# Optimization experiments

Measured on AMD Instinct MI355X. Metric: run time of the kernel, lower is better.

Reference implementation:

```python
import jax, jax.numpy as jnp
import numpy as np

RMS_EPS = 1e-5
L2_EPS = 1e-8


def _rms_norm(x, eps=RMS_EPS):
    return x * jax.lax.rsqrt(jnp.mean(x * x, axis=-1, keepdims=True) + eps)


def _l2_norm(x, eps=L2_EPS):
    return jnp.linalg.norm(x, ord=2, axis=-1, keepdims=True) + eps


def setup_inputs() -> dict:
    key = jax.random.key(0)
    kq, kk, kv = jax.random.split(key, 3)
    B, H, S, D = 4, 16, 4096, 64
    Q = jax.random.normal(kq, (B, H, S, D), dtype=jnp.float32)
    K = jax.random.normal(kk, (B, H, S, D), dtype=jnp.float32)
    V = jax.random.normal(kv, (B, H, S, D), dtype=jnp.float32)
    return {"Q": Q, "K": K, "V": V}


def reference(Q, K, V):
    # v_swiglu = SiLU(V) * V
    v_swiglu = jax.nn.silu(V) * V
    # causal cumulative sum over sequence dim
    c = jnp.cumsum(v_swiglu, axis=-2)
    c_n = _rms_norm(c)
    # gating scalar per (b,h,s): ||Q|| + ||K|| + 1
    r = _l2_norm(Q) + _l2_norm(K) + 1.0
    mstate = c_n / r
    # SwiGLU combine: V + SiLU(mstate) * V, then final RMSNorm
    out0 = V + jax.nn.silu(mstate) * V
    return _rms_norm(out0)
```

## Files before the change

kernel.cpp:

```cpp
#include <hip/hip_runtime.h>
#include <math.h>

#define BH 64
#define SEQ 4096
#define DIM 64
#define CHUNK 32
#define NCHUNK (SEQ / CHUNK)
#define WPB 4

__device__ __forceinline__ float fast_rcp(float x)  { return __builtin_amdgcn_rcpf(x); }
__device__ __forceinline__ float fast_rsqrt(float x){ return __builtin_amdgcn_rsqf(x); }
__device__ __forceinline__ float fast_sigmoid(float x) {
    return fast_rcp(1.0f + __expf(-x));
}


__global__ __launch_bounds__(256) void k_partials(const float* __restrict__ Q,
                                                  const float* __restrict__ K,
                                                  const float* __restrict__ V,
                                                  float* __restrict__ P,
                                                  float* __restrict__ R) {
    const int wave  = threadIdx.x >> 6;
    const int lane  = threadIdx.x & 63;
    const int g     = lane >> 4;
    const int h     = lane & 15;
    const int chunk = blockIdx.x * WPB + wave;

    const size_t cbase = (size_t)chunk * (CHUNK * DIM);
    const float4* q4 = (const float4*)(Q + cbase);
    const float4* k4 = (const float4*)(K + cbase);
    const float4* v4 = (const float4*)(V + cbase);

    float acc0 = 0.f, acc1 = 0.f, acc2 = 0.f, acc3 = 0.f;

#pragma unroll
    for (int j0 = 0; j0 < CHUNK; j0 += 4) {
        const int row = j0 + g;
        const int idx = row * 16 + h;
        float4 q = q4[idx];
        float4 k = k4[idx];
        float4 v = v4[idx];

        float q2 = q.x*q.x + q.y*q.y + q.z*q.z + q.w*q.w;
        float k2 = k.x*k.x + k.y*k.y + k.z*k.z + k.w*k.w;
#pragma unroll
        for (int m = 1; m < 16; m <<= 1) {
            q2 += __shfl_xor(q2, m);
            k2 += __shfl_xor(k2, m);
        }
        float r = sqrtf(q2) + sqrtf(k2) + 1.0f;
        if (h == 0) R[(size_t)chunk * CHUNK + row] = r;

        acc0 += v.x * v.x * fast_sigmoid(v.x);
        acc1 += v.y * v.y * fast_sigmoid(v.y);
        acc2 += v.z * v.z * fast_sigmoid(v.z);
        acc3 += v.w * v.w * fast_sigmoid(v.w);
    }

#pragma unroll
    for (int m = 16; m < 64; m <<= 1) {
        acc0 += __shfl_xor(acc0, m);
        acc1 += __shfl_xor(acc1, m);
        acc2 += __shfl_xor(acc2, m);
        acc3 += __shfl_xor(acc3, m);
    }
    if (g == 0) {
        float4 out = {acc0, acc1, acc2, acc3};
        ((float4*)(P + (size_t)chunk * DIM))[h] = out;
    }
}

__global__ __launch_bounds__(256) void k_prefix(float* __restrict__ P) {
    __shared__ float seg[WPB][DIM];
    const int wave = threadIdx.x >> 6;
    const int lane = threadIdx.x & 63;
    const int bh   = blockIdx.x;
    const int SEG  = NCHUNK / WPB;

    float* p = P + (size_t)bh * (NCHUNK * DIM) + (size_t)wave * SEG * DIM + lane;

    float t[SEG];
#pragma unroll
    for (int i = 0; i < SEG; ++i) t[i] = p[i * DIM];

    float run = 0.f;
#pragma unroll
    for (int i = 0; i < SEG; ++i) { float x = t[i]; t[i] = run; run += x; }

    seg[wave][lane] = run;
    __syncthreads();

    float carry = 0.f;
#pragma unroll
    for (int w = 0; w < WPB; ++w)
        if (w < wave) carry += seg[w][lane];

#pragma unroll
    for (int i = 0; i < SEG; ++i) p[i * DIM] = t[i] + carry;
}

__global__ __launch_bounds__(256) void k_scan(const float* __restrict__ V,
                                              const float* __restrict__ P,
                                              const float* __restrict__ R,
                                              float* __restrict__ O) {
    const int wave  = threadIdx.x >> 6;
    const int lane  = threadIdx.x & 63;
    const int g     = lane >> 4;
    const int h     = lane & 15;
    const int chunk = blockIdx.x * WPB + wave;

    const size_t cbase = (size_t)chunk * (CHUNK * DIM);
    const float4* v4 = (const float4*)(V + cbase);
    float4*       o4 = (float4*)(O + cbase);
    const float*  rp = R + (size_t)chunk * CHUNK;

    float4 cb = ((const float4*)(P + (size_t)chunk * DIM))[h];
    float c_base[4] = {cb.x, cb.y, cb.z, cb.w};

    const int up16 = (lane + 48) & 63;
    const int up32 = (lane + 32) & 63;
    const int src3 = 48 + h;

#pragma unroll
    for (int j0 = 0; j0 < CHUNK; j0 += 4) {
        const int row = j0 + g;
        float4 v = v4[row * 16 + h];

        float sw[4];
        sw[0] = v.x * v.x * fast_sigmoid(v.x);
        sw[1] = v.y * v.y * fast_sigmoid(v.y);
        sw[2] = v.z * v.z * fast_sigmoid(v.z);
        sw[3] = v.w * v.w * fast_sigmoid(v.w);

#pragma unroll
        for (int i = 0; i < 4; ++i) {
            float t = __shfl(sw[i], up16);
            sw[i] += (g >= 1) ? t : 0.f;
        }
#pragma unroll
        for (int i = 0; i < 4; ++i) {
            float t = __shfl(sw[i], up32);
            sw[i] += (g >= 2) ? t : 0.f;
        }

        float c_row[4], tot[4];
#pragma unroll
        for (int i = 0; i < 4; ++i) {
            tot[i]   = __shfl(sw[i], src3);
            c_row[i] = c_base[i] + sw[i];
            c_base[i] += tot[i];
        }

        float c2 = c_row[0]*c_row[0] + c_row[1]*c_row[1]
                 + c_row[2]*c_row[2] + c_row[3]*c_row[3];
#pragma unroll
        for (int m = 1; m < 16; m <<= 1) c2 += __shfl_xor(c2, m);

        float r     = rp[row];
        float rms_c = fast_rsqrt(c2 * (1.0f / 64.0f) + 1e-5f);
        float s     = rms_c * fast_rcp(r);

        float vv[4] = {v.x, v.y, v.z, v.w};
        float o[4];
#pragma unroll
        for (int i = 0; i < 4; ++i) {
            float m_ = c_row[i] * s;
            o[i] = vv[i] * (1.0f + m_ * fast_sigmoid(m_));
        }

        float o2 = o[0]*o[0] + o[1]*o[1] + o[2]*o[2] + o[3]*o[3];
#pragma unroll
        for (int m = 1; m < 16; m <<= 1) o2 += __shfl_xor(o2, m);

        float rms_o = fast_rsqrt(o2 * (1.0f / 64.0f) + 1e-5f);
        float4 out = {o[0]*rms_o, o[1]*rms_o, o[2]*rms_o, o[3]*rms_o};
        o4[row * 16 + h] = out;
    }
}

extern "C" void kernel_launch(void* const* d_in, const int* in_sizes, int n_in,
                              void* d_out, int out_size, void* d_ws, size_t ws_size,
                              hipStream_t stream) {
    const float* Q = (const float*)d_in[0];
    const float* K = (const float*)d_in[1];
    const float* V = (const float*)d_in[2];
    float* O = (float*)d_out;
    float* P = (float*)d_ws;
    float* R = (float*)d_ws + (size_t)BH * NCHUNK * DIM;

    const int nchunks = BH * NCHUNK;
    k_partials<<<nchunks / WPB, 256, 0, stream>>>(Q, K, V, P, R);
    k_prefix<<<BH, 256, 0, stream>>>(P);
    k_scan<<<nchunks / WPB, 256, 0, stream>>>(V, P, R, O);
}
```

Baseline: 234.5 us.

## Fuse three-pass scan into persistent kernel with grid barriers

Replaces the partials, prefix and scan kernels with one persistent kernel of 256 blocks that uses two atomic grid-wide barriers between phases. Each wave handles several chunks. The Q/K norm computation moves from the partials pass into the final pass, so the R buffer round trip goes away and Q/K are read only once. The aim is to remove kernel launch gaps and the R traffic. In exchange it adds a memset, spin-wait barriers that rely on all 256 blocks being co-resident, and less parallelism per phase.

```diff
diff --git a/kernel.cpp b/kernel.cpp
--- a/kernel.cpp
+++ b/kernel.cpp
@@ -6,7 +6,12 @@
 #define DIM 64
 #define CHUNK 32
 #define NCHUNK (SEQ / CHUNK)
-#define WPB 4
+#define TPB 512
+#define WPB 8
+#define BLOCKS 256
+#define TOTAL_WAVES (BLOCKS * WPB)
+#define CPW ((BH * NCHUNK) / TOTAL_WAVES)
+#define PFX_SEG (NCHUNK / WPB)
 
 __device__ __forceinline__ float fast_rcp(float x)  { return __builtin_amdgcn_rcpf(x); }
 __device__ __forceinline__ float fast_rsqrt(float x){ return __builtin_amdgcn_rsqf(x); }
@@ -14,167 +19,172 @@
     return fast_rcp(1.0f + __expf(-x));
 }
 
-
-__global__ __launch_bounds__(256) void k_partials(const float* __restrict__ Q,
+__device__ __forceinline__ void grid_barrier(int* cnt, int* flag) {
+    __syncthreads();
+    __threadfence();
+    if (threadIdx.x == 0) {
+        int prev = atomicAdd(cnt, 1);
+        if (prev == BLOCKS - 1) {
+            atomicExch(flag, 1);
+        } else {
+            while (atomicAdd(flag, 0) == 0) {
+                __builtin_amdgcn_s_sleep(8);
+            }
+        }
+    }
+    __syncthreads();
+    __threadfence();
+}
+
+__global__ __launch_bounds__(TPB, 4) void k_fused(const float* __restrict__ Q,
                                                   const float* __restrict__ K,
                                                   const float* __restrict__ V,
                                                   float* __restrict__ P,
-                                                  float* __restrict__ R) {
-    const int wave  = threadIdx.x >> 6;
-    const int lane  = threadIdx.x & 63;
-    const int g     = lane >> 4;
-    const int h     = lane & 15;
-    const int chunk = blockIdx.x * WPB + wave;
-
-    const size_t cbase = (size_t)chunk * (CHUNK * DIM);
-    const float4* q4 = (const float4*)(Q + cbase);
-    const float4* k4 = (const float4*)(K + cbase);
-    const float4* v4 = (const float4*)(V + cbase);
-
-    float acc0 = 0.f, acc1 = 0.f, acc2 = 0.f, acc3 = 0.f;
-
-#pragma unroll
-    for (int j0 = 0; j0 < CHUNK; j0 += 4) {
-        const int row = j0 + g;
-        const int idx = row * 16 + h;
-        float4 q = q4[idx];
-        float4 k = k4[idx];
-        float4 v = v4[idx];
-
-        float q2 = q.x*q.x + q.y*q.y + q.z*q.z + q.w*q.w;
-        float k2 = k.x*k.x + k.y*k.y + k.z*k.z + k.w*k.w;
-#pragma unroll
-        for (int m = 1; m < 16; m <<= 1) {
-            q2 += __shfl_xor(q2, m);
-            k2 += __shfl_xor(k2, m);
-        }
-        float r = sqrtf(q2) + sqrtf(k2) + 1.0f;
-        if (h == 0) R[(size_t)chunk * CHUNK + row] = r;
-
-        acc0 += v.x * v.x * fast_sigmoid(v.x);
-        acc1 += v.y * v.y * fast_sigmoid(v.y);
-        acc2 += v.z * v.z * fast_sigmoid(v.z);
-        acc3 += v.w * v.w * fast_sigmoid(v.w);
-    }
-
-#pragma unroll
-    for (int m = 16; m < 64; m <<= 1) {
-        acc0 += __shfl_xor(acc0, m);
-        acc1 += __shfl_xor(acc1, m);
-        acc2 += __shfl_xor(acc2, m);
-        acc3 += __shfl_xor(acc3, m);
-    }
-    if (g == 0) {
-        float4 out = {acc0, acc1, acc2, acc3};
-        ((float4*)(P + (size_t)chunk * DIM))[h] = out;
-    }
-}
-
-__global__ __launch_bounds__(256) void k_prefix(float* __restrict__ P) {
+                                                  float* __restrict__ O,
+                                                  int* __restrict__ bar) {
     __shared__ float seg[WPB][DIM];
+
     const int wave = threadIdx.x >> 6;
     const int lane = threadIdx.x & 63;
-    const int bh   = blockIdx.x;
-    const int SEG  = NCHUNK / WPB;
-
-    float* p = P + (size_t)bh * (NCHUNK * DIM) + (size_t)wave * SEG * DIM + lane;
-
-    float t[SEG];
-#pragma unroll
-    for (int i = 0; i < SEG; ++i) t[i] = p[i * DIM];
-
-    float run = 0.f;
-#pragma unroll
-    for (int i = 0; i < SEG; ++i) { float x = t[i]; t[i] = run; run += x; }
-
-    seg[wave][lane] = run;
-    __syncthreads();
-
-    float carry = 0.f;
-#pragma unroll
-    for (int w = 0; w < WPB; ++w)
-        if (w < wave) carry += seg[w][lane];
-
-#pragma unroll
-    for (int i = 0; i < SEG; ++i) p[i * DIM] = t[i] + carry;
-}
-
-__global__ __launch_bounds__(256) void k_scan(const float* __restrict__ V,
-                                              const float* __restrict__ P,
-                                              const float* __restrict__ R,
-                                              float* __restrict__ O) {
-    const int wave  = threadIdx.x >> 6;
-    const int lane  = threadIdx.x & 63;
-    const int g     = lane >> 4;
-    const int h     = lane & 15;
-    const int chunk = blockIdx.x * WPB + wave;
-
-    const size_t cbase = (size_t)chunk * (CHUNK * DIM);
-    const float4* v4 = (const float4*)(V + cbase);
-    float4*       o4 = (float4*)(O + cbase);
-    const float*  rp = R + (size_t)chunk * CHUNK;
-
-    float4 cb = ((const float4*)(P + (size_t)chunk * DIM))[h];
-    float c_base[4] = {cb.x, cb.y, cb.z, cb.w};
+    const int g    = lane >> 4;
+    const int h    = lane & 15;
+    const int wid  = blockIdx.x * WPB + wave;
+
+    for (int t = 0; t < CPW; ++t) {
+        const int chunk = wid * CPW + t;
+        const float4* v4 = (const float4*)(V + (size_t)chunk * (CHUNK * DIM));
+
+        float acc0 = 0.f, acc1 = 0.f, acc2 = 0.f, acc3 = 0.f;
+#pragma unroll
+        for (int j0 = 0; j0 < CHUNK; j0 += 4) {
+            float4 v = v4[(j0 + g) * 16 + h];
+            acc0 += v.x * v.x * fast_sigmoid(v.x);
+            acc1 += v.y * v.y * fast_sigmoid(v.y);
+            acc2 += v.z * v.z * fast_sigmoid(v.z);
+            acc3 += v.w * v.w * fast_sigmoid(v.w);
+        }
+#pragma unroll
+        for (int m = 16; m < 64; m <<= 1) {
+            acc0 += __shfl_xor(acc0, m);
+            acc1 += __shfl_xor(acc1, m);
+            acc2 += __shfl_xor(acc2, m);
+            acc3 += __shfl_xor(acc3, m);
+        }
+        if (g == 0) {
+            float4 out = {acc0, acc1, acc2, acc3};
+            ((float4*)(P + (size_t)chunk * DIM))[h] = out;
+        }
+    }
+
+    grid_barrier(bar + 0, bar + 1);
+
+    if (blockIdx.x < BH) {
+        const int bh = blockIdx.x;
+        float* p = P + (size_t)bh * (NCHUNK * DIM) + (size_t)wave * PFX_SEG * DIM + lane;
+
+        float tr[PFX_SEG];
+#pragma unroll
+        for (int i = 0; i < PFX_SEG; ++i) tr[i] = p[i * DIM];
+
+        float run = 0.f;
+#pragma unroll
+        for (int i = 0; i < PFX_SEG; ++i) { float x = tr[i]; tr[i] = run; run += x; }
+
+        seg[wave][lane] = run;
+        __syncthreads();
+
+        float carry = 0.f;
+#pragma unroll
+        for (int w = 0; w < WPB; ++w)
+            if (w < wave) carry += seg[w][lane];
+
+#pragma unroll
+        for (int i = 0; i < PFX_SEG; ++i) p[i * DIM] = tr[i] + carry;
+    }
+
+    grid_barrier(bar + 2, bar + 3);
 
     const int up16 = (lane + 48) & 63;
     const int up32 = (lane + 32) & 63;
     const int src3 = 48 + h;
 
-#pragma unroll
-    for (int j0 = 0; j0 < CHUNK; j0 += 4) {
-        const int row = j0 + g;
-        float4 v = v4[row * 16 + h];
-
-        float sw[4];
-        sw[0] = v.x * v.x * fast_sigmoid(v.x);
-        sw[1] = v.y * v.y * fast_sigmoid(v.y);
-        sw[2] = v.z * v.z * fast_sigmoid(v.z);
-        sw[3] = v.w * v.w * fast_sigmoid(v.w);
-
-#pragma unroll
-        for (int i = 0; i < 4; ++i) {
-            float t = __shfl(sw[i], up16);
-            sw[i] += (g >= 1) ? t : 0.f;
-        }
-#pragma unroll
-        for (int i = 0; i < 4; ++i) {
-            float t = __shfl(sw[i], up32);
-            sw[i] += (g >= 2) ? t : 0.f;
-        }
-
-        float c_row[4], tot[4];
-#pragma unroll
-        for (int i = 0; i < 4; ++i) {
-            tot[i]   = __shfl(sw[i], src3);
-            c_row[i] = c_base[i] + sw[i];
-            c_base[i] += tot[i];
-        }
-
-        float c2 = c_row[0]*c_row[0] + c_row[1]*c_row[1]
-                 + c_row[2]*c_row[2] + c_row[3]*c_row[3];
-#pragma unroll
-        for (int m = 1; m < 16; m <<= 1) c2 += __shfl_xor(c2, m);
-
-        float r     = rp[row];
-        float rms_c = fast_rsqrt(c2 * (1.0f / 64.0f) + 1e-5f);
-        float s     = rms_c * fast_rcp(r);
-
-        float vv[4] = {v.x, v.y, v.z, v.w};
-        float o[4];
-#pragma unroll
-        for (int i = 0; i < 4; ++i) {
-            float m_ = c_row[i] * s;
-            o[i] = vv[i] * (1.0f + m_ * fast_sigmoid(m_));
-        }
-
-        float o2 = o[0]*o[0] + o[1]*o[1] + o[2]*o[2] + o[3]*o[3];
-#pragma unroll
-        for (int m = 1; m < 16; m <<= 1) o2 += __shfl_xor(o2, m);
-
-        float rms_o = fast_rsqrt(o2 * (1.0f / 64.0f) + 1e-5f);
-        float4 out = {o[0]*rms_o, o[1]*rms_o, o[2]*rms_o, o[3]*rms_o};
-        o4[row * 16 + h] = out;
+    for (int t = 0; t < CPW; ++t) {
+        const int chunk = wid * CPW + t;
+        const size_t cbase = (size_t)chunk * (CHUNK * DIM);
+        const float4* q4 = (const float4*)(Q + cbase);
+        const float4* k4 = (const float4*)(K + cbase);
+        const float4* v4 = (const float4*)(V + cbase);
+        float4*       o4 = (float4*)(O + cbase);
+
+        float4 cb = ((const float4*)(P + (size_t)chunk * DIM))[h];
+        float c_base[4] = {cb.x, cb.y, cb.z, cb.w};
+
+#pragma unroll
+        for (int j0 = 0; j0 < CHUNK; j0 += 4) {
+            const int row = j0 + g;
+            const int idx = row * 16 + h;
+            float4 v = v4[idx];
+            float4 q = q4[idx];
+            float4 k = k4[idx];
+
+            float q2 = q.x*q.x + q.y*q.y + q.z*q.z + q.w*q.w;
+            float k2 = k.x*k.x + k.y*k.y + k.z*k.z + k.w*k.w;
+#pragma unroll
+            for (int m = 1; m < 16; m <<= 1) {
+                q2 += __shfl_xor(q2, m);
+                k2 += __shfl_xor(k2, m);
+            }
+            float r = sqrtf(q2) + sqrtf(k2) + 1.0f;
+
+            float sw[4];
+            sw[0] = v.x * v.x * fast_sigmoid(v.x);
+            sw[1] = v.y * v.y * fast_sigmoid(v.y);
+            sw[2] = v.z * v.z * fast_sigmoid(v.z);
+            sw[3] = v.w * v.w * fast_sigmoid(v.w);
+
+#pragma unroll
+            for (int i = 0; i < 4; ++i) {
+                float tt = __shfl(sw[i], up16);
+                sw[i] += (g >= 1) ? tt : 0.f;
+            }
+#pragma unroll
+            for (int i = 0; i < 4; ++i) {
+                float tt = __shfl(sw[i], up32);
+                sw[i] += (g >= 2) ? tt : 0.f;
+            }
+
+            float c_row[4];
+#pragma unroll
+            for (int i = 0; i < 4; ++i) {
+                float tot = __shfl(sw[i], src3);
+                c_row[i]  = c_base[i] + sw[i];
+                c_base[i] += tot;
+            }
+
+            float c2 = c_row[0]*c_row[0] + c_row[1]*c_row[1]
+                     + c_row[2]*c_row[2] + c_row[3]*c_row[3];
+#pragma unroll
+            for (int m = 1; m < 16; m <<= 1) c2 += __shfl_xor(c2, m);
+
+            float rms_c = fast_rsqrt(c2 * (1.0f / 64.0f) + 1e-5f);
+            float s     = rms_c * fast_rcp(r);
+
+            float vv[4] = {v.x, v.y, v.z, v.w};
+            float o[4];
+#pragma unroll
+            for (int i = 0; i < 4; ++i) {
+                float m_ = c_row[i] * s;
+                o[i] = vv[i] * (1.0f + m_ * fast_sigmoid(m_));
+            }
+
+            float o2 = o[0]*o[0] + o[1]*o[1] + o[2]*o[2] + o[3]*o[3];
+#pragma unroll
+            for (int m = 1; m < 16; m <<= 1) o2 += __shfl_xor(o2, m);
+
+            float rms_o = fast_rsqrt(o2 * (1.0f / 64.0f) + 1e-5f);
+            float4 out = {o[0]*rms_o, o[1]*rms_o, o[2]*rms_o, o[3]*rms_o};
+            o4[idx] = out;
+        }
     }
 }
 
@@ -186,10 +196,8 @@
     const float* V = (const float*)d_in[2];
     float* O = (float*)d_out;
     float* P = (float*)d_ws;
-    float* R = (float*)d_ws + (size_t)BH * NCHUNK * DIM;
-
-    const int nchunks = BH * NCHUNK;
-    k_partials<<<nchunks / WPB, 256, 0, stream>>>(Q, K, V, P, R);
-    k_prefix<<<BH, 256, 0, stream>>>(P);
-    k_scan<<<nchunks / WPB, 256, 0, stream>>>(V, P, R, O);
-}
+    int* bar = (int*)((char*)d_ws + (size_t)BH * NCHUNK * DIM * sizeof(float));
+
+    hipMemsetAsync(bar, 0, 4 * sizeof(int), stream);
+    k_fused<<<BLOCKS, TPB, 0, stream>>>(Q, K, V, P, O, bar);
+}
```

After: 371.2 us. 1.58x slower.

## Fuse prefix pass into scan kernel and move Q/K norm computation there

Applied to the files above, without the earlier changes.

Drops the separate prefix kernel: each scan block recomputes the chunk-prefix carry for its batch-head slab from the partial sums, using shared memory. The Q/K L2-norm gate is now computed inside the scan kernel instead of the partials kernel, so the R buffer round trip goes away and the partials pass reads only V. Each wave now handles two chunks, interleaved, to expose more memory-level parallelism, with launch bounds set for occupancy. The cost is redundant prefix reads of P in every block (16 blocks per slab) and more registers per thread.

```diff
diff --git a/kernel.cpp b/kernel.cpp
--- a/kernel.cpp
+++ b/kernel.cpp
@@ -6,7 +6,10 @@
 #define DIM 64
 #define CHUNK 32
 #define NCHUNK (SEQ / CHUNK)
-#define WPB 4
+#define NCH_TOT (BH * NCHUNK)
+#define P1_WPB 4
+#define CPB 8
+#define SBLOCKS (NCH_TOT / CPB)
 
 __device__ __forceinline__ float fast_rcp(float x)  { return __builtin_amdgcn_rcpf(x); }
 __device__ __forceinline__ float fast_rsqrt(float x){ return __builtin_amdgcn_rsqf(x); }
@@ -14,108 +17,161 @@
     return fast_rcp(1.0f + __expf(-x));
 }
 
+__device__ __forceinline__ float red16(float x) {
+    x += __shfl_xor(x, 1);
+    x += __shfl_xor(x, 2);
+    x += __shfl_xor(x, 4);
+    x += __shfl_xor(x, 8);
+    return x;
+}
 
-__global__ __launch_bounds__(256) void k_partials(const float* __restrict__ Q,
-                                                  const float* __restrict__ K,
-                                                  const float* __restrict__ V,
-                                                  float* __restrict__ P,
-                                                  float* __restrict__ R) {
-    const int wave  = threadIdx.x >> 6;
-    const int lane  = threadIdx.x & 63;
-    const int g     = lane >> 4;
-    const int h     = lane & 15;
-    const int chunk = blockIdx.x * WPB + wave;
+__global__ __launch_bounds__(256) void k_partials(const float* __restrict__ V,
+                                                  float* __restrict__ P) {
+    const int wave = threadIdx.x >> 6;
+    const int lane = threadIdx.x & 63;
+    const int g = lane >> 4, h = lane & 15;
+    const int chunk = blockIdx.x * P1_WPB + wave;
 
-    const size_t cbase = (size_t)chunk * (CHUNK * DIM);
-    const float4* q4 = (const float4*)(Q + cbase);
-    const float4* k4 = (const float4*)(K + cbase);
-    const float4* v4 = (const float4*)(V + cbase);
-
-    float acc0 = 0.f, acc1 = 0.f, acc2 = 0.f, acc3 = 0.f;
-
+    const float4* v4 = (const float4*)(V + (size_t)chunk * (CHUNK * DIM));
+    float a0 = 0.f, a1 = 0.f, a2 = 0.f, a3 = 0.f;
 #pragma unroll
     for (int j0 = 0; j0 < CHUNK; j0 += 4) {
-        const int row = j0 + g;
-        const int idx = row * 16 + h;
-        float4 q = q4[idx];
-        float4 k = k4[idx];
-        float4 v = v4[idx];
-
-        float q2 = q.x*q.x + q.y*q.y + q.z*q.z + q.w*q.w;
-        float k2 = k.x*k.x + k.y*k.y + k.z*k.z + k.w*k.w;
-#pragma unroll
-        for (int m = 1; m < 16; m <<= 1) {
-            q2 += __shfl_xor(q2, m);
-            k2 += __shfl_xor(k2, m);
-        }
-        float r = sqrtf(q2) + sqrtf(k2) + 1.0f;
-        if (h == 0) R[(size_t)chunk * CHUNK + row] = r;
-
-        acc0 += v.x * v.x * fast_sigmoid(v.x);
-        acc1 += v.y * v.y * fast_sigmoid(v.y);
-        acc2 += v.z * v.z * fast_sigmoid(v.z);
-        acc3 += v.w * v.w * fast_sigmoid(v.w);
+        float4 v = v4[(j0 + g) * 16 + h];
+        a0 += v.x * v.x * fast_sigmoid(v.x);
+        a1 += v.y * v.y * fast_sigmoid(v.y);
+        a2 += v.z * v.z * fast_sigmoid(v.z);
+        a3 += v.w * v.w * fast_sigmoid(v.w);
     }
-
 #pragma unroll
     for (int m = 16; m < 64; m <<= 1) {
-        acc0 += __shfl_xor(acc0, m);
-        acc1 += __shfl_xor(acc1, m);
-        acc2 += __shfl_xor(acc2, m);
-        acc3 += __shfl_xor(acc3, m);
+        a0 += __shfl_xor(a0, m);
+        a1 += __shfl_xor(a1, m);
+        a2 += __shfl_xor(a2, m);
+        a3 += __shfl_xor(a3, m);
     }
     if (g == 0) {
-        float4 out = {acc0, acc1, acc2, acc3};
-        ((float4*)(P + (size_t)chunk * DIM))[h] = out;
+        float4 o = {a0, a1, a2, a3};
+        ((float4*)(P + (size_t)chunk * DIM))[h] = o;
     }
 }
 
-__global__ __launch_bounds__(256) void k_prefix(float* __restrict__ P) {
-    __shared__ float seg[WPB][DIM];
-    const int wave = threadIdx.x >> 6;
-    const int lane = threadIdx.x & 63;
-    const int bh   = blockIdx.x;
-    const int SEG  = NCHUNK / WPB;
+__device__ __forceinline__ void scan_step(const float4* __restrict__ q4,
+                                          const float4* __restrict__ k4,
+                                          const float4* __restrict__ v4,
+                                          float4* __restrict__ o4,
+                                          float (&cb)[4],
+                                          int idx, int g,
+                                          int up16, int up32, int src3) {
+    float4 v = v4[idx];
+    float4 q = q4[idx];
+    float4 k = k4[idx];
 
-    float* p = P + (size_t)bh * (NCHUNK * DIM) + (size_t)wave * SEG * DIM + lane;
+    float q2 = red16(q.x*q.x + q.y*q.y + q.z*q.z + q.w*q.w);
+    float k2 = red16(k.x*k.x + k.y*k.y + k.z*k.z + k.w*k.w);
+    float r  = sqrtf(q2) + sqrtf(k2) + 1.0f;
 
-    float t[SEG];
+    float s0 = v.x * v.x * fast_sigmoid(v.x);
+    float s1 = v.y * v.y * fast_sigmoid(v.y);
+    float s2v = v.z * v.z * fast_sigmoid(v.z);
+    float s3 = v.w * v.w * fast_sigmoid(v.w);
+
+    float t0 = __shfl(s0, up16); s0 += (g >= 1) ? t0 : 0.f;
+    float t1 = __shfl(s1, up16); s1 += (g >= 1) ? t1 : 0.f;
+    float t2 = __shfl(s2v, up16); s2v += (g >= 1) ? t2 : 0.f;
+    float t3 = __shfl(s3, up16); s3 += (g >= 1) ? t3 : 0.f;
+
+    float u0 = __shfl(s0, up32); s0 += (g >= 2) ? u0 : 0.f;
+    float u1 = __shfl(s1, up32); s1 += (g >= 2) ? u1 : 0.f;
+    float u2 = __shfl(s2v, up32); s2v += (g >= 2) ? u2 : 0.f;
+    float u3 = __shfl(s3, up32); s3 += (g >= 2) ? u3 : 0.f;
+
+    float w0 = __shfl(s0, src3);
+    float w1 = __shfl(s1, src3);
+    float w2 = __shfl(s2v, src3);
+    float w3 = __shfl(s3, src3);
+
+    float c0 = cb[0] + s0;  cb[0] += w0;
+    float c1 = cb[1] + s1;  cb[1] += w1;
+    float c2 = cb[2] + s2v; cb[2] += w2;
+    float c3 = cb[3] + s3;  cb[3] += w3;
+
+    float cs = red16(c0*c0 + c1*c1 + c2*c2 + c3*c3);
+    float rms_c = fast_rsqrt(cs * (1.0f / 64.0f) + 1e-5f);
+    float s = rms_c * fast_rcp(r);
+
+    float m0 = c0 * s; float o0 = v.x * (1.0f + m0 * fast_sigmoid(m0));
+    float m1 = c1 * s; float o1 = v.y * (1.0f + m1 * fast_sigmoid(m1));
+    float m2 = c2 * s; float o2 = v.z * (1.0f + m2 * fast_sigmoid(m2));
+    float m3 = c3 * s; float o3 = v.w * (1.0f + m3 * fast_sigmoid(m3));
+
+    float os = red16(o0*o0 + o1*o1 + o2*o2 + o3*o3);
+    float rms_o = fast_rsqrt(os * (1.0f / 64.0f) + 1e-5f);
+    float4 outv = {o0 * rms_o, o1 * rms_o, o2 * rms_o, o3 * rms_o};
+    o4[idx] = outv;
+}
+
+__global__ __launch_bounds__(256, 4) void k_scan(const float* __restrict__ Q,
+                                                 const float* __restrict__ K,
+                                                 const float* __restrict__ V,
+                                                 const float* __restrict__ P,
+                                                 float* __restrict__ O) {
+    __shared__ float segsum[4][DIM];
+    __shared__ float excl[CPB][DIM];
+
+    const int t    = threadIdx.x;
+    const int lane = t & 63;
+    const int wave = t >> 6;
+    const int b    = blockIdx.x;
+    const int bib  = b & 15;
+    const float* pslab = P + (size_t)(b >> 4) * (NCHUNK * DIM);
+
+    float run = 0.f, run8 = 0.f, run16 = 0.f, run24 = 0.f;
 #pragma unroll
-    for (int i = 0; i < SEG; ++i) t[i] = p[i * DIM];
-
-    float run = 0.f;
-#pragma unroll
-    for (int i = 0; i < SEG; ++i) { float x = t[i]; t[i] = run; run += x; }
-
-    seg[wave][lane] = run;
+    for (int j = 0; j < 32; ++j) {
+        if (j == 8)  run8  = run;
+        if (j == 16) run16 = run;
+        if (j == 24) run24 = run;
+        run += pslab[(wave * 32 + j) * DIM + lane];
+    }
+    segsum[wave][lane] = run;
     __syncthreads();
 
-    float carry = 0.f;
+    const int seg_t = bib >> 2;
+    const int off   = (bib & 3) * 8;
+    if (wave == seg_t) {
+        float carry = 0.f;
 #pragma unroll
-    for (int w = 0; w < WPB; ++w)
-        if (w < wave) carry += seg[w][lane];
+        for (int s = 0; s < 4; ++s)
+            if (s < seg_t) carry += segsum[s][lane];
+        float ws = carry + (off == 0 ? 0.f :
+                            off == 8 ? run8 :
+                            off == 16 ? run16 : run24);
+#pragma unroll
+        for (int i = 0; i < CPB; ++i) {
+            excl[i][lane] = ws;
+            ws += pslab[(seg_t * 32 + off + i) * DIM + lane];
+        }
+    }
+    __syncthreads();
 
-#pragma unroll
-    for (int i = 0; i < SEG; ++i) p[i * DIM] = t[i] + carry;
-}
+    const int g = lane >> 4, h = lane & 15;
+    const int cA = b * CPB + 2 * wave;
+    const int cB = cA + 1;
+    const size_t baseA = (size_t)cA * (CHUNK * DIM);
+    const size_t baseB = (size_t)cB * (CHUNK * DIM);
+    const float4* qA = (const float4*)(Q + baseA);
+    const float4* kA = (const float4*)(K + baseA);
+    const float4* vA = (const float4*)(V + baseA);
+    float4*       oA = (float4*)(O + baseA);
+    const float4* qB = (const float4*)(Q + baseB);
+    const float4* kB = (const float4*)(K + baseB);
+    const float4* vB = (const float4*)(V + baseB);
+    float4*       oB = (float4*)(O + baseB);
 
-__global__ __launch_bounds__(256) void k_scan(const float* __restrict__ V,
-                                              const float* __restrict__ P,
-                                              const float* __restrict__ R,
-                                              float* __restrict__ O) {
-    const int wave  = threadIdx.x >> 6;
-    const int lane  = threadIdx.x & 63;
-    const int g     = lane >> 4;
-    const int h     = lane & 15;
-    const int chunk = blockIdx.x * WPB + wave;
-
-    const size_t cbase = (size_t)chunk * (CHUNK * DIM);
-    const float4* v4 = (const float4*)(V + cbase);
-    float4*       o4 = (float4*)(O + cbase);
-    const float*  rp = R + (size_t)chunk * CHUNK;
-
-    float4 cb = ((const float4*)(P + (size_t)chunk * DIM))[h];
-    float c_base[4] = {cb.x, cb.y, cb.z, cb.w};
+    float4 ea = ((const float4*)excl[2 * wave])[h];
+    float4 eb = ((const float4*)excl[2 * wave + 1])[h];
+    float cbA[4] = {ea.x, ea.y, ea.z, ea.w};
+    float cbB[4] = {eb.x, eb.y, eb.z, eb.w};
 
     const int up16 = (lane + 48) & 63;
     const int up32 = (lane + 32) & 63;
@@ -123,58 +179,9 @@
 
 #pragma unroll
     for (int j0 = 0; j0 < CHUNK; j0 += 4) {
-        const int row = j0 + g;
-        float4 v = v4[row * 16 + h];
-
-        float sw[4];
-        sw[0] = v.x * v.x * fast_sigmoid(v.x);
-        sw[1] = v.y * v.y * fast_sigmoid(v.y);
-        sw[2] = v.z * v.z * fast_sigmoid(v.z);
-        sw[3] = v.w * v.w * fast_sigmoid(v.w);
-
-#pragma unroll
-        for (int i = 0; i < 4; ++i) {
-            float t = __shfl(sw[i], up16);
-            sw[i] += (g >= 1) ? t : 0.f;
-        }
-#pragma unroll
-        for (int i = 0; i < 4; ++i) {
-            float t = __shfl(sw[i], up32);
-            sw[i] += (g >= 2) ? t : 0.f;
-        }
-
-        float c_row[4], tot[4];
-#pragma unroll
-        for (int i = 0; i < 4; ++i) {
-            tot[i]   = __shfl(sw[i], src3);
-            c_row[i] = c_base[i] + sw[i];
-            c_base[i] += tot[i];
-        }
-
-        float c2 = c_row[0]*c_row[0] + c_row[1]*c_row[1]
-                 + c_row[2]*c_row[2] + c_row[3]*c_row[3];
-#pragma unroll
-        for (int m = 1; m < 16; m <<= 1) c2 += __shfl_xor(c2, m);
-
-        float r     = rp[row];
-        float rms_c = fast_rsqrt(c2 * (1.0f / 64.0f) + 1e-5f);
-        float s     = rms_c * fast_rcp(r);
-
-        float vv[4] = {v.x, v.y, v.z, v.w};
-        float o[4];
-#pragma unroll
-        for (int i = 0; i < 4; ++i) {
-            float m_ = c_row[i] * s;
-            o[i] = vv[i] * (1.0f + m_ * fast_sigmoid(m_));
-        }
-
-        float o2 = o[0]*o[0] + o[1]*o[1] + o[2]*o[2] + o[3]*o[3];
-#pragma unroll
-        for (int m = 1; m < 16; m <<= 1) o2 += __shfl_xor(o2, m);
-
-        float rms_o = fast_rsqrt(o2 * (1.0f / 64.0f) + 1e-5f);
-        float4 out = {o[0]*rms_o, o[1]*rms_o, o[2]*rms_o, o[3]*rms_o};
-        o4[row * 16 + h] = out;
+        const int idx = (j0 + g) * 16 + h;
+        scan_step(qA, kA, vA, oA, cbA, idx, g, up16, up32, src3);
+        scan_step(qB, kB, vB, oB, cbB, idx, g, up16, up32, src3);
     }
 }
 
@@ -186,10 +193,7 @@
     const float* V = (const float*)d_in[2];
     float* O = (float*)d_out;
     float* P = (float*)d_ws;
-    float* R = (float*)d_ws + (size_t)BH * NCHUNK * DIM;
 
-    const int nchunks = BH * NCHUNK;
-    k_partials<<<nchunks / WPB, 256, 0, stream>>>(Q, K, V, P, R);
-    k_prefix<<<BH, 256, 0, stream>>>(P);
-    k_scan<<<nchunks / WPB, 256, 0, stream>>>(V, P, R, O);
+    k_partials<<<NCH_TOT / P1_WPB, 256, 0, stream>>>(V, P);
+    k_scan<<<SBLOCKS, 256, 0, stream>>>(Q, K, V, P, O);
 }
```

Result: faster. 225.1 us (-4.0%).
